# Kernel optimization log

Hardware: AMD Instinct MI355X
Metric: run time of the kernel (lower is better)

Reference implementation:

```python
import jax, jax.numpy as jnp
import numpy as np

B, N, D_MODEL = 8, 1024, 512
H, DK = 8, 64
STATIONS = 128
MASK_NEG = -1e9
LN_EPS = 1e-6


def setup_inputs() -> dict:
    key = jax.random.key(0)
    ks = jax.random.split(key, 9)
    return {
        "hidden_states": jax.random.normal(ks[0], (B, N, D_MODEL), dtype=jnp.float32),
        "rpe": jax.random.normal(ks[1], (B, H, N, N), dtype=jnp.float32) * 0.1,
        "Wq": jax.random.normal(ks[2], (H * DK, D_MODEL), dtype=jnp.float32) * 0.02,
        "Wk": jax.random.normal(ks[3], (H * DK, D_MODEL), dtype=jnp.float32) * 0.02,
        "Wv": jax.random.normal(ks[4], (H * DK, D_MODEL), dtype=jnp.float32) * 0.02,
        "fc_w": jax.random.normal(ks[5], (D_MODEL, H * DK), dtype=jnp.float32) * 0.02,
        "fc_b": jnp.zeros((D_MODEL,), dtype=jnp.float32),
        "ln_g": jnp.ones((D_MODEL,), dtype=jnp.float32),
        "ln_b": jnp.zeros((D_MODEL,), dtype=jnp.float32),
    }


def _star_mask(n, stations):
    # q_k_mask: query i attends to key j iff j < stations or i == j
    idx = jnp.arange(n)
    return (idx[None, :] < stations) | (idx[:, None] == idx[None, :])  # [n, n] bool


def reference(hidden_states, rpe, Wq, Wk, Wv, fc_w, fc_b, ln_g, ln_b):
    b, n, _ = hidden_states.shape
    residual = hidden_states
    q = (hidden_states @ Wq.T).reshape(b, n, H, DK)
    k = (hidden_states @ Wk.T).reshape(b, n, H, DK)
    v = (hidden_states @ Wv.T).reshape(b, n, H, DK)
    # sparse star+self-loop QK^T with inline RPE add (dense emulation of QKP_mm_tvm)
    scores = jnp.einsum("bihd,bjhd->bhij", q, k) + rpe  # [b,h,n,n]
    mask = _star_mask(n, STATIONS)
    scores = jnp.where(mask[None, None], scores, MASK_NEG)
    scores = scores / jnp.sqrt(jnp.float32(DK))
    attn = jax.nn.softmax(scores, axis=-1)
    # AttnV_mm_tvm: sparse attn-weights times V
    ctx = jnp.einsum("bhij,bjhd->bihd", attn, v).reshape(b, n, H * DK)
    ctx = ctx @ fc_w.T + fc_b + residual
    mu = jnp.mean(ctx, axis=-1, keepdims=True)
    var = jnp.var(ctx, axis=-1, keepdims=True)
    return (ctx - mu) / jnp.sqrt(var + LN_EPS) * ln_g + ln_b
```

## Files before the change

kernel.cpp:

```cpp
#include <hip/hip_runtime.h>
#include <hip/hip_bf16.h>
#include <math.h>

#define B_  8
#define N_  1024
#define DM  512
#define H_  8
#define DK_ 64
#define ST  128

typedef __attribute__((ext_vector_type(8))) short short8;
typedef __attribute__((ext_vector_type(4))) float floatx4;

#define GLD16(gp, lp)                                                          \
    __builtin_amdgcn_global_load_lds(                                          \
        (const __attribute__((address_space(1))) void*)(gp),                   \
        (__attribute__((address_space(3))) void*)(lp), 16, 0, 0)

__device__ __forceinline__ float b2f(short u) {
    union { unsigned int i; float f; } c;
    c.i = ((unsigned int)(unsigned short)u) << 16;
    return c.f;
}
__device__ __forceinline__ unsigned short f2b(float f) {
    __hip_bfloat16 t = __float2bfloat16(f);
    return *(unsigned short*)&t;
}

struct CastArgs {
    const float* src[5];
    unsigned short* dst[5];
    int n[5];
};

__global__ __launch_bounds__(256)
void cast_bf16_kernel(CastArgs a)
{
    const int j = blockIdx.y;
    const float* __restrict__ s = a.src[j];
    unsigned short* __restrict__ d = a.dst[j];
    const int n = a.n[j];
    int i = (blockIdx.x * 256 + threadIdx.x) * 8;
    if (i >= n) return;
    float4 x0 = *(const float4*)&s[i];
    float4 x1 = *(const float4*)&s[i + 4];
    ushort4 o0, o1;
    o0.x = f2b(x0.x); o0.y = f2b(x0.y); o0.z = f2b(x0.z); o0.w = f2b(x0.w);
    o1.x = f2b(x1.x); o1.y = f2b(x1.y); o1.z = f2b(x1.z); o1.w = f2b(x1.w);
    *(ushort4*)&d[i] = o0;
    *(ushort4*)&d[i + 4] = o1;
}

__device__ __forceinline__
void gemm_core(const unsigned short* __restrict__ A,
               const unsigned short* __restrict__ W,
               int m0, int n0, unsigned short* As, unsigned short* Bs,
               floatx4 acc[4][4])
{
    const int tid = threadIdx.x;
    const int lane = tid & 63;
    const int wave = tid >> 6;
    const int wm = wave >> 1, wn = wave & 1;
    const int srow = tid >> 2;
    const int skq  = (tid & 3) * 8;
    const unsigned short* Ag = A + (size_t)(m0 + srow) * 512 + skq;
    const unsigned short* Bg = W + (size_t)(n0 + srow) * 512 + skq;
    const int mrow = lane & 15;
    const int koff = (lane >> 4) * 8;

    for (int kt = 0; kt < 512; kt += 32) {
        __syncthreads();
        GLD16(Ag + kt,            &As[tid * 8]);
        GLD16(Ag + 64 * 512 + kt, &As[2048 + tid * 8]);
        GLD16(Bg + kt,            &Bs[tid * 8]);
        GLD16(Bg + 64 * 512 + kt, &Bs[2048 + tid * 8]);
        __syncthreads();
        short8 af[4], bf[4];
        #pragma unroll
        for (int t = 0; t < 4; ++t) {
            af[t] = *(const short8*)&As[(wm * 64 + t * 16 + mrow) * 32 + koff];
            bf[t] = *(const short8*)&Bs[(wn * 64 + t * 16 + mrow) * 32 + koff];
        }
        #pragma unroll
        for (int mt = 0; mt < 4; ++mt)
            #pragma unroll
            for (int nt = 0; nt < 4; ++nt)
                acc[mt][nt] = __builtin_amdgcn_mfma_f32_16x16x32_bf16(
                    af[mt], bf[nt], acc[mt][nt], 0, 0, 0);
    }
}

__global__ __launch_bounds__(256)
void qkv_gemm_kernel(const unsigned short* __restrict__ A,
                     const unsigned short* __restrict__ W0,
                     const unsigned short* __restrict__ W1,
                     const unsigned short* __restrict__ W2,
                     unsigned short* __restrict__ qo,
                     unsigned short* __restrict__ ko,
                     unsigned short* __restrict__ vto)
{
    __shared__ __align__(16) unsigned short As[128 * 32];
    __shared__ __align__(16) unsigned short Bs[128 * 32];
    const int by = blockIdx.y;
    const int sel = by >> 2;
    const unsigned short* W = (sel == 0) ? W0 : (sel == 1 ? W1 : W2);
    const int m0 = blockIdx.x * 128;
    const int n0 = (by & 3) * 128;

    floatx4 acc[4][4];
    #pragma unroll
    for (int i = 0; i < 4; ++i)
        #pragma unroll
        for (int j = 0; j < 4; ++j)
            acc[i][j] = (floatx4){0.f, 0.f, 0.f, 0.f};

    gemm_core(A, W, m0, n0, As, Bs, acc);

    const int lane = threadIdx.x & 63;
    const int wave = threadIdx.x >> 6;
    const int wm = wave >> 1, wn = wave & 1;
    const int lx = lane & 15;
    const int rq = (lane >> 4) * 4;

    if (sel == 2) {
        #pragma unroll
        for (int mt = 0; mt < 4; ++mt) {
            const int mrow = m0 + wm * 64 + mt * 16 + rq;
            const int bb = mrow >> 10, tok = mrow & 1023;
            #pragma unroll
            for (int nt = 0; nt < 4; ++nt) {
                const int c = n0 + wn * 64 + nt * 16 + lx;
                const int hh = c >> 6, d = c & 63;
                ushort4 pk;
                pk.x = f2b(acc[mt][nt][0]); pk.y = f2b(acc[mt][nt][1]);
                pk.z = f2b(acc[mt][nt][2]); pk.w = f2b(acc[mt][nt][3]);
                *(ushort4*)&vto[((size_t)(bb * H_ + hh) * DK_ + d) * N_ + tok] = pk;
            }
        }
    } else {
        unsigned short* O = (sel == 0) ? qo : ko;
        #pragma unroll
        for (int mt = 0; mt < 4; ++mt) {
            const int mrow = m0 + wm * 64 + mt * 16 + rq;
            const int bb = mrow >> 10, tok = mrow & 1023;
            #pragma unroll
            for (int nt = 0; nt < 4; ++nt) {
                const int c = n0 + wn * 64 + nt * 16 + lx;
                const int hh = c >> 6, d = c & 63;
                unsigned short* p =
                    O + ((size_t)(bb * H_ + hh) * N_ + tok) * DK_ + d;
                #pragma unroll
                for (int r = 0; r < 4; ++r)
                    p[(size_t)r * DK_] = f2b(acc[mt][nt][r]);
            }
        }
    }
}

__global__ __launch_bounds__(256)
void fc_gemm_kernel(const unsigned short* __restrict__ A,
                    const unsigned short* __restrict__ W,
                    const float* __restrict__ bias,
                    const float* __restrict__ resid,
                    float* __restrict__ C)
{
    __shared__ __align__(16) unsigned short As[128 * 32];
    __shared__ __align__(16) unsigned short Bs[128 * 32];
    const int m0 = blockIdx.x * 128;
    const int n0 = blockIdx.y * 128;

    floatx4 acc[4][4];
    #pragma unroll
    for (int i = 0; i < 4; ++i)
        #pragma unroll
        for (int j = 0; j < 4; ++j)
            acc[i][j] = (floatx4){0.f, 0.f, 0.f, 0.f};

    gemm_core(A, W, m0, n0, As, Bs, acc);

    const int lane = threadIdx.x & 63;
    const int wave = threadIdx.x >> 6;
    const int wm = wave >> 1, wn = wave & 1;
    const int col = n0 + wn * 64 + (lane & 15);
    const int rq  = (lane >> 4) * 4;
    #pragma unroll
    for (int mt = 0; mt < 4; ++mt)
        #pragma unroll
        for (int nt = 0; nt < 4; ++nt) {
            const int c = col + nt * 16;
            const float b = bias[c];
            #pragma unroll
            for (int r = 0; r < 4; ++r) {
                const size_t row = (size_t)(m0 + wm * 64 + mt * 16 + rq + r);
                C[row * 512 + c] = acc[mt][nt][r] + b + resid[row * 512 + c];
            }
        }
}

__global__ __launch_bounds__(256)
void attn_kernel(const unsigned short* __restrict__ qg,
                 const unsigned short* __restrict__ kg,
                 const unsigned short* __restrict__ vtg,
                 const float* __restrict__ rpe,
                 unsigned short* __restrict__ ctx)
{
    __shared__ __align__(16) unsigned short P[64 * 136];

    const int tid  = threadIdx.x;
    const int lane = tid & 63;
    const int w    = tid >> 6;
    const int lx   = lane & 15;
    const int quad = lane >> 4;
    const int qb = blockIdx.x * 64;
    const int h  = blockIdx.y, b = blockIdx.z;
    const int bh = b * H_ + h;
    const unsigned short* qh  = qg  + (size_t)bh * N_ * DK_;
    const unsigned short* kh  = kg  + (size_t)bh * N_ * DK_;
    const unsigned short* vth = vtg + (size_t)bh * DK_ * N_;
    const float* rp = rpe + ((size_t)bh * N_ + qb) * N_;
    const bool has_self = (qb >= ST);

    float sself = -1e30f;
    if (has_self) {
        const int i = qb + w * 16 + lx;
        const unsigned short* qr = qh + (size_t)i * DK_ + quad * 16;
        const unsigned short* kr = kh + (size_t)i * DK_ + quad * 16;
        short8 q0 = *(const short8*)qr, q1 = *(const short8*)(qr + 8);
        short8 k0 = *(const short8*)kr, k1 = *(const short8*)(kr + 8);
        float dot = 0.f;
        #pragma unroll
        for (int j = 0; j < 8; ++j) {
            dot = fmaf(b2f(q0[j]), b2f(k0[j]), dot);
            dot = fmaf(b2f(q1[j]), b2f(k1[j]), dot);
        }
        dot += __shfl_xor(dot, 16, 64);
        dot += __shfl_xor(dot, 32, 64);
        const float rd = rp[(size_t)(w * 16 + lx) * N_ + (qb + w * 16 + lx)];
        sself = (dot + rd) * 0.125f;
    }

    float rv[4][8];
    {
        const float* rbase = rp + (size_t)(w * 16 + quad * 4) * N_ + lx;
        #pragma unroll
        for (int r = 0; r < 4; ++r)
            #pragma unroll
            for (int nt = 0; nt < 8; ++nt)
                rv[r][nt] = rbase[(size_t)r * N_ + nt * 16];
    }

    short8 aq[2];
    {
        const unsigned short* qrow =
            qh + (size_t)(qb + w * 16 + lx) * DK_ + quad * 8;
        aq[0] = *(const short8*)qrow;
        aq[1] = *(const short8*)(qrow + 32);
    }
    floatx4 sacc[8];
    #pragma unroll
    for (int nt = 0; nt < 8; ++nt) sacc[nt] = (floatx4){0.f, 0.f, 0.f, 0.f};
    #pragma unroll
    for (int nt = 0; nt < 8; ++nt) {
        const unsigned short* krow =
            kh + (size_t)(nt * 16 + lx) * DK_ + quad * 8;
        short8 b0 = *(const short8*)krow;
        short8 b1 = *(const short8*)(krow + 32);
        sacc[nt] = __builtin_amdgcn_mfma_f32_16x16x32_bf16(aq[0], b0, sacc[nt], 0, 0, 0);
        sacc[nt] = __builtin_amdgcn_mfma_f32_16x16x32_bf16(aq[1], b1, sacc[nt], 0, 0, 0);
    }

    float l4[4], ps4[4];
    #pragma unroll
    for (int r = 0; r < 4; ++r) {
        float sv[8];
        float mx = -1e30f;
        #pragma unroll
        for (int nt = 0; nt < 8; ++nt) {
            sv[nt] = (sacc[nt][r] + rv[r][nt]) * 0.125f;
            mx = fmaxf(mx, sv[nt]);
        }
        #pragma unroll
        for (int o = 1; o < 16; o <<= 1)
            mx = fmaxf(mx, __shfl_xor(mx, o, 64));
        const float ss = __shfl(sself, quad * 4 + r, 64);
        mx = fmaxf(mx, ss);
        float sum = 0.f;
        #pragma unroll
        for (int nt = 0; nt < 8; ++nt) {
            sv[nt] = __expf(sv[nt] - mx);
            sum += sv[nt];
        }
        #pragma unroll
        for (int o = 1; o < 16; o <<= 1)
            sum += __shfl_xor(sum, o, 64);
        const float ps = has_self ? __expf(ss - mx) : 0.f;
        l4[r] = sum + ps;
        ps4[r] = ps;
        const int row = w * 16 + quad * 4 + r;
        #pragma unroll
        for (int nt = 0; nt < 8; ++nt)
            P[row * 136 + nt * 16 + lx] = f2b(sv[nt]);
    }
    __syncthreads();

    short8 ap[4];
    #pragma unroll
    for (int ks = 0; ks < 4; ++ks)
        ap[ks] = *(const short8*)&P[(w * 16 + lx) * 136 + ks * 32 + quad * 8];
    floatx4 oacc[4];
    #pragma unroll
    for (int nt = 0; nt < 4; ++nt) oacc[nt] = (floatx4){0.f, 0.f, 0.f, 0.f};
    #pragma unroll
    for (int nt = 0; nt < 4; ++nt) {
        const unsigned short* vrow = vth + (size_t)(nt * 16 + lx) * N_;
        #pragma unroll
        for (int ks = 0; ks < 4; ++ks) {
            short8 bv = *(const short8*)(vrow + ks * 32 + quad * 8);
            oacc[nt] = __builtin_amdgcn_mfma_f32_16x16x32_bf16(ap[ks], bv, oacc[nt], 0, 0, 0);
        }
    }

    #pragma unroll
    for (int r = 0; r < 4; ++r) {
        const int i = qb + w * 16 + quad * 4 + r;
        const float inv = 1.0f / l4[r];
        const float ps = ps4[r];
        #pragma unroll
        for (int nt = 0; nt < 4; ++nt) {
            const int d = nt * 16 + lx;
            float o = oacc[nt][r];
            if (has_self)
                o = fmaf(ps, b2f((short)vth[(size_t)d * N_ + i]), o);
            ctx[((size_t)(b * N_) + i) * DM + h * DK_ + d] = f2b(o * inv);
        }
    }
}

__global__ __launch_bounds__(256)
void ln_kernel(float* __restrict__ io, const float* __restrict__ g,
               const float* __restrict__ bb)
{
    const int t = blockIdx.x;
    const int tid = threadIdx.x;
    float* row = io + (size_t)t * DM;
    float2 x = *(const float2*)&row[tid * 2];
    float s  = x.x + x.y;
    float ss = fmaf(x.x, x.x, x.y * x.y);
    #pragma unroll
    for (int o = 1; o < 64; o <<= 1) {
        s  += __shfl_xor(s,  o, 64);
        ss += __shfl_xor(ss, o, 64);
    }
    __shared__ float wsum[4], wsq[4];
    const int w = tid >> 6;
    if ((tid & 63) == 0) { wsum[w] = s; wsq[w] = ss; }
    __syncthreads();
    s  = wsum[0] + wsum[1] + wsum[2] + wsum[3];
    ss = wsq[0]  + wsq[1]  + wsq[2]  + wsq[3];
    const float mean = s * (1.0f / DM);
    const float var  = ss * (1.0f / DM) - mean * mean;
    const float rstd = rsqrtf(var + 1e-6f);
    float2 gg = *(const float2*)&g[tid * 2];
    float2 bv = *(const float2*)&bb[tid * 2];
    x.x = (x.x - mean) * rstd * gg.x + bv.x;
    x.y = (x.y - mean) * rstd * gg.y + bv.y;
    *(float2*)&row[tid * 2] = x;
}

extern "C" void kernel_launch(void* const* d_in, const int* in_sizes, int n_in,
                              void* d_out, int out_size, void* d_ws, size_t ws_size,
                              hipStream_t stream)
{
    (void)in_sizes; (void)n_in; (void)out_size; (void)ws_size;
    const float* hidden = (const float*)d_in[0];
    const float* rpe    = (const float*)d_in[1];
    const float* Wq     = (const float*)d_in[2];
    const float* Wk     = (const float*)d_in[3];
    const float* Wv     = (const float*)d_in[4];
    const float* fc_w   = (const float*)d_in[5];
    const float* fc_b   = (const float*)d_in[6];
    const float* ln_g   = (const float*)d_in[7];
    const float* ln_b   = (const float*)d_in[8];
    float* out = (float*)d_out;
    char* ws = (char*)d_ws;

    const size_t MB = 1024 * 1024;
    unsigned short* hb  = (unsigned short*)(ws + 0 * MB);
    unsigned short* wq  = (unsigned short*)(ws + 8 * MB);
    unsigned short* wk  = (unsigned short*)(ws + 8 * MB + 512 * 1024);
    unsigned short* wv  = (unsigned short*)(ws + 9 * MB);
    unsigned short* wf  = (unsigned short*)(ws + 9 * MB + 512 * 1024);
    unsigned short* qB  = (unsigned short*)(ws + 16 * MB);
    unsigned short* kB  = (unsigned short*)(ws + 24 * MB);
    unsigned short* vtB = (unsigned short*)(ws + 32 * MB);
    unsigned short* cb  = (unsigned short*)(ws + 40 * MB);

    CastArgs ca;
    ca.src[0] = hidden; ca.dst[0] = hb; ca.n[0] = B_ * N_ * DM;
    ca.src[1] = Wq;     ca.dst[1] = wq; ca.n[1] = DM * DM;
    ca.src[2] = Wk;     ca.dst[2] = wk; ca.n[2] = DM * DM;
    ca.src[3] = Wv;     ca.dst[3] = wv; ca.n[3] = DM * DM;
    ca.src[4] = fc_w;   ca.dst[4] = wf; ca.n[4] = DM * DM;
    cast_bf16_kernel<<<dim3(2048, 5), 256, 0, stream>>>(ca);

    qkv_gemm_kernel<<<dim3(64, 12), 256, 0, stream>>>(hb, wq, wk, wv, qB, kB, vtB);
    attn_kernel<<<dim3(16, H_, B_), 256, 0, stream>>>(qB, kB, vtB, rpe, cb);
    fc_gemm_kernel<<<dim3(64, 4), 256, 0, stream>>>(cb, wf, fc_b, hidden, out);
    ln_kernel<<<B_ * N_, 256, 0, stream>>>(out, ln_g, ln_b);
}
```

Measured before the change: 400.2 us.

## Fuse output projection with LayerNorm and double GEMM K-tile depth

Merges the fc GEMM, bias, residual add and LayerNorm into one kernel. Each block computes a full 32-row by 512-column output tile, reduces row statistics across waves in shared memory, and writes normalized output once. This removes the intermediate fp32 round trip and one launch. The fused kernel reads weights straight from global memory without LDS staging and launches only 256 blocks, which may lower occupancy and reuse. Separately, the shared GEMM core now stages K=64 per iteration instead of 32, halving barrier count at the cost of doubled LDS per block.

```diff
diff --git a/kernel.cpp b/kernel.cpp
--- a/kernel.cpp
+++ b/kernel.cpp
@@ -61,32 +61,41 @@
     const int lane = tid & 63;
     const int wave = tid >> 6;
     const int wm = wave >> 1, wn = wave & 1;
-    const int srow = tid >> 2;
-    const int skq  = (tid & 3) * 8;
-    const unsigned short* Ag = A + (size_t)(m0 + srow) * 512 + skq;
-    const unsigned short* Bg = W + (size_t)(n0 + srow) * 512 + skq;
+    const int r0 = tid >> 3;
+    const int k0 = (tid & 7) * 8;
+    const unsigned short* Ag = A + (size_t)(m0 + r0) * 512 + k0;
+    const unsigned short* Bg = W + (size_t)(n0 + r0) * 512 + k0;
     const int mrow = lane & 15;
     const int koff = (lane >> 4) * 8;
 
-    for (int kt = 0; kt < 512; kt += 32) {
+    for (int kt = 0; kt < 512; kt += 64) {
         __syncthreads();
         GLD16(Ag + kt,            &As[tid * 8]);
-        GLD16(Ag + 64 * 512 + kt, &As[2048 + tid * 8]);
+        GLD16(Ag + 32 * 512 + kt, &As[2048 + tid * 8]);
+        GLD16(Ag + 64 * 512 + kt, &As[4096 + tid * 8]);
+        GLD16(Ag + 96 * 512 + kt, &As[6144 + tid * 8]);
         GLD16(Bg + kt,            &Bs[tid * 8]);
-        GLD16(Bg + 64 * 512 + kt, &Bs[2048 + tid * 8]);
+        GLD16(Bg + 32 * 512 + kt, &Bs[2048 + tid * 8]);
+        GLD16(Bg + 64 * 512 + kt, &Bs[4096 + tid * 8]);
+        GLD16(Bg + 96 * 512 + kt, &Bs[6144 + tid * 8]);
         __syncthreads();
-        short8 af[4], bf[4];
-        #pragma unroll
-        for (int t = 0; t < 4; ++t) {
-            af[t] = *(const short8*)&As[(wm * 64 + t * 16 + mrow) * 32 + koff];
-            bf[t] = *(const short8*)&Bs[(wn * 64 + t * 16 + mrow) * 32 + koff];
-        }
-        #pragma unroll
-        for (int mt = 0; mt < 4; ++mt)
-            #pragma unroll
-            for (int nt = 0; nt < 4; ++nt)
-                acc[mt][nt] = __builtin_amdgcn_mfma_f32_16x16x32_bf16(
-                    af[mt], bf[nt], acc[mt][nt], 0, 0, 0);
+        #pragma unroll
+        for (int ks = 0; ks < 2; ++ks) {
+            short8 af[4], bf[4];
+            #pragma unroll
+            for (int t = 0; t < 4; ++t) {
+                af[t] = *(const short8*)
+                    &As[(wm * 64 + t * 16 + mrow) * 64 + ks * 32 + koff];
+                bf[t] = *(const short8*)
+                    &Bs[(wn * 64 + t * 16 + mrow) * 64 + ks * 32 + koff];
+            }
+            #pragma unroll
+            for (int mt = 0; mt < 4; ++mt)
+                #pragma unroll
+                for (int nt = 0; nt < 4; ++nt)
+                    acc[mt][nt] = __builtin_amdgcn_mfma_f32_16x16x32_bf16(
+                        af[mt], bf[nt], acc[mt][nt], 0, 0, 0);
+        }
     }
 }
 
@@ -99,8 +108,8 @@
                      unsigned short* __restrict__ ko,
                      unsigned short* __restrict__ vto)
 {
-    __shared__ __align__(16) unsigned short As[128 * 32];
-    __shared__ __align__(16) unsigned short Bs[128 * 32];
+    __shared__ __align__(16) unsigned short As[128 * 64];
+    __shared__ __align__(16) unsigned short Bs[128 * 64];
     const int by = blockIdx.y;
     const int sel = by >> 2;
     const unsigned short* W = (sel == 0) ? W0 : (sel == 1 ? W1 : W2);
@@ -155,46 +164,6 @@
             }
         }
     }
-}
-
-__global__ __launch_bounds__(256)
-void fc_gemm_kernel(const unsigned short* __restrict__ A,
-                    const unsigned short* __restrict__ W,
-                    const float* __restrict__ bias,
-                    const float* __restrict__ resid,
-                    float* __restrict__ C)
-{
-    __shared__ __align__(16) unsigned short As[128 * 32];
-    __shared__ __align__(16) unsigned short Bs[128 * 32];
-    const int m0 = blockIdx.x * 128;
-    const int n0 = blockIdx.y * 128;
-
-    floatx4 acc[4][4];
-    #pragma unroll
-    for (int i = 0; i < 4; ++i)
-        #pragma unroll
-        for (int j = 0; j < 4; ++j)
-            acc[i][j] = (floatx4){0.f, 0.f, 0.f, 0.f};
-
-    gemm_core(A, W, m0, n0, As, Bs, acc);
-
-    const int lane = threadIdx.x & 63;
-    const int wave = threadIdx.x >> 6;
-    const int wm = wave >> 1, wn = wave & 1;
-    const int col = n0 + wn * 64 + (lane & 15);
-    const int rq  = (lane >> 4) * 4;
-    #pragma unroll
-    for (int mt = 0; mt < 4; ++mt)
-        #pragma unroll
-        for (int nt = 0; nt < 4; ++nt) {
-            const int c = col + nt * 16;
-            const float b = bias[c];
-            #pragma unroll
-            for (int r = 0; r < 4; ++r) {
-                const size_t row = (size_t)(m0 + wm * 64 + mt * 16 + rq + r);
-                C[row * 512 + c] = acc[mt][nt][r] + b + resid[row * 512 + c];
-            }
-        }
 }
 
 __global__ __launch_bounds__(256)
@@ -337,34 +306,123 @@
 }
 
 __global__ __launch_bounds__(256)
-void ln_kernel(float* __restrict__ io, const float* __restrict__ g,
-               const float* __restrict__ bb)
-{
-    const int t = blockIdx.x;
-    const int tid = threadIdx.x;
-    float* row = io + (size_t)t * DM;
-    float2 x = *(const float2*)&row[tid * 2];
-    float s  = x.x + x.y;
-    float ss = fmaf(x.x, x.x, x.y * x.y);
-    #pragma unroll
-    for (int o = 1; o < 64; o <<= 1) {
-        s  += __shfl_xor(s,  o, 64);
-        ss += __shfl_xor(ss, o, 64);
-    }
-    __shared__ float wsum[4], wsq[4];
-    const int w = tid >> 6;
-    if ((tid & 63) == 0) { wsum[w] = s; wsq[w] = ss; }
+void fc_ln_kernel(const unsigned short* __restrict__ A,
+                  const unsigned short* __restrict__ W,
+                  const float* __restrict__ bias,
+                  const float* __restrict__ resid,
+                  const float* __restrict__ g,
+                  const float* __restrict__ bb,
+                  float* __restrict__ out)
+{
+    __shared__ __align__(16) unsigned short As[32 * 64];
+    __shared__ float Ssum[32][4], Ssq[32][4];
+    __shared__ float Smean[32], Srstd[32];
+
+    const int tid  = threadIdx.x;
+    const int lane = tid & 63;
+    const int w    = tid >> 6;
+    const int lx   = lane & 15;
+    const int quad = lane >> 4;
+    const int m0 = blockIdx.x * 32;
+
+    const int r0 = tid >> 3;
+    const int k0 = (tid & 7) * 8;
+    const unsigned short* Ag = A + (size_t)(m0 + r0) * 512 + k0;
+    const int koff = quad * 8;
+
+    floatx4 acc[2][8];
+    #pragma unroll
+    for (int mt = 0; mt < 2; ++mt)
+        #pragma unroll
+        for (int ct = 0; ct < 8; ++ct)
+            acc[mt][ct] = (floatx4){0.f, 0.f, 0.f, 0.f};
+
+    for (int kt = 0; kt < 512; kt += 64) {
+        __syncthreads();
+        GLD16(Ag + kt, &As[tid * 8]);
+        __syncthreads();
+        #pragma unroll
+        for (int ks = 0; ks < 2; ++ks) {
+            short8 af0 = *(const short8*)&As[(lx) * 64 + ks * 32 + koff];
+            short8 af1 = *(const short8*)&As[(16 + lx) * 64 + ks * 32 + koff];
+            #pragma unroll
+            for (int ct = 0; ct < 8; ++ct) {
+                const int col = w * 128 + ct * 16 + lx;
+                short8 bv = *(const short8*)
+                    &W[(size_t)col * 512 + kt + ks * 32 + koff];
+                acc[0][ct] = __builtin_amdgcn_mfma_f32_16x16x32_bf16(
+                    af0, bv, acc[0][ct], 0, 0, 0);
+                acc[1][ct] = __builtin_amdgcn_mfma_f32_16x16x32_bf16(
+                    af1, bv, acc[1][ct], 0, 0, 0);
+            }
+        }
+    }
+
+    float bias_c[8];
+    #pragma unroll
+    for (int ct = 0; ct < 8; ++ct)
+        bias_c[ct] = bias[w * 128 + ct * 16 + lx];
+
+    float sum[2][4], sq[2][4];
+    #pragma unroll
+    for (int mt = 0; mt < 2; ++mt)
+        #pragma unroll
+        for (int r = 0; r < 4; ++r) {
+            const int row = m0 + mt * 16 + quad * 4 + r;
+            float s = 0.f, q2 = 0.f;
+            #pragma unroll
+            for (int ct = 0; ct < 8; ++ct) {
+                float vvv = acc[mt][ct][r] + bias_c[ct]
+                    + resid[(size_t)row * 512 + w * 128 + ct * 16 + lx];
+                acc[mt][ct][r] = vvv;
+                s += vvv;
+                q2 = fmaf(vvv, vvv, q2);
+            }
+            #pragma unroll
+            for (int o = 1; o < 16; o <<= 1) {
+                s  += __shfl_xor(s,  o, 64);
+                q2 += __shfl_xor(q2, o, 64);
+            }
+            sum[mt][r] = s; sq[mt][r] = q2;
+        }
+    if (lx == 0) {
+        #pragma unroll
+        for (int mt = 0; mt < 2; ++mt)
+            #pragma unroll
+            for (int r = 0; r < 4; ++r) {
+                Ssum[mt * 16 + quad * 4 + r][w] = sum[mt][r];
+                Ssq [mt * 16 + quad * 4 + r][w] = sq[mt][r];
+            }
+    }
     __syncthreads();
-    s  = wsum[0] + wsum[1] + wsum[2] + wsum[3];
-    ss = wsq[0]  + wsq[1]  + wsq[2]  + wsq[3];
-    const float mean = s * (1.0f / DM);
-    const float var  = ss * (1.0f / DM) - mean * mean;
-    const float rstd = rsqrtf(var + 1e-6f);
-    float2 gg = *(const float2*)&g[tid * 2];
-    float2 bv = *(const float2*)&bb[tid * 2];
-    x.x = (x.x - mean) * rstd * gg.x + bv.x;
-    x.y = (x.y - mean) * rstd * gg.y + bv.y;
-    *(float2*)&row[tid * 2] = x;
+    if (tid < 32) {
+        float s  = Ssum[tid][0] + Ssum[tid][1] + Ssum[tid][2] + Ssum[tid][3];
+        float q2 = Ssq[tid][0]  + Ssq[tid][1]  + Ssq[tid][2]  + Ssq[tid][3];
+        const float mean = s * (1.0f / DM);
+        const float var  = q2 * (1.0f / DM) - mean * mean;
+        Smean[tid] = mean;
+        Srstd[tid] = rsqrtf(var + 1e-6f);
+    }
+    __syncthreads();
+
+    float gv[8], bv2[8];
+    #pragma unroll
+    for (int ct = 0; ct < 8; ++ct) {
+        const int col = w * 128 + ct * 16 + lx;
+        gv[ct] = g[col]; bv2[ct] = bb[col];
+    }
+    #pragma unroll
+    for (int mt = 0; mt < 2; ++mt)
+        #pragma unroll
+        for (int r = 0; r < 4; ++r) {
+            const int lrow = mt * 16 + quad * 4 + r;
+            const int row  = m0 + lrow;
+            const float mean = Smean[lrow], rstd = Srstd[lrow];
+            #pragma unroll
+            for (int ct = 0; ct < 8; ++ct)
+                out[(size_t)row * 512 + w * 128 + ct * 16 + lx] =
+                    (acc[mt][ct][r] - mean) * rstd * gv[ct] + bv2[ct];
+        }
 }
 
 extern "C" void kernel_launch(void* const* d_in, const int* in_sizes, int n_in,
@@ -405,6 +463,5 @@
 
     qkv_gemm_kernel<<<dim3(64, 12), 256, 0, stream>>>(hb, wq, wk, wv, qB, kB, vtB);
     attn_kernel<<<dim3(16, H_, B_), 256, 0, stream>>>(qB, kB, vtB, rpe, cb);
-    fc_gemm_kernel<<<dim3(64, 4), 256, 0, stream>>>(cb, wf, fc_b, hidden, out);
-    ln_kernel<<<B_ * N_, 256, 0, stream>>>(out, ln_g, ln_b);
-}
+    fc_ln_kernel<<<256, 256, 0, stream>>>(cb, wf, fc_b, hidden, ln_g, ln_b, out);
+}
```

Measured after the change: 411.5 us. 1.03x slower.
